# Kernel tuning notes

Measured on AMD Instinct MI355X. Metric: run time of the kernel, lower is better.

The kernel has to match this reference:

```python
import jax, jax.numpy as jnp
import numpy as np

D_MODEL = 1024
N_HEADS = 16
D_K = D_MODEL // N_HEADS
B, T = 4, 2048


def setup_inputs() -> dict:
    key = jax.random.key(0)
    ks = jax.random.split(key, 6)
    scale = 1.0 / np.sqrt(D_MODEL)
    q = jax.random.normal(ks[0], (B, T, D_MODEL), dtype=jnp.float32)
    # causal mask: True = masked / ignored (upper triangle)
    causal = jnp.triu(jnp.ones((T, T), dtype=bool), k=1)
    mask = jnp.broadcast_to(causal, (B, 1, T, T))
    Wq = jax.random.normal(ks[1], (D_MODEL, D_MODEL), dtype=jnp.float32) * scale
    Wk = jax.random.normal(ks[2], (D_MODEL, D_MODEL), dtype=jnp.float32) * scale
    Wv = jax.random.normal(ks[3], (D_MODEL, D_MODEL), dtype=jnp.float32) * scale
    Wo = jax.random.normal(ks[4], (D_MODEL, D_MODEL), dtype=jnp.float32) * scale
    bq = jnp.zeros((D_MODEL,), jnp.float32)
    bk = jnp.zeros((D_MODEL,), jnp.float32)
    bv = jnp.zeros((D_MODEL,), jnp.float32)
    bo = jnp.zeros((D_MODEL,), jnp.float32)
    return {"q": q, "mask": mask, "Wq": Wq, "bq": bq, "Wk": Wk, "bk": bk,
            "Wv": Wv, "bv": bv, "Wo": Wo, "bo": bo}


def reference(q, mask, Wq, bq, Wk, bk, Wv, bv, Wo, bo):
    # Self-attention: k = v = q (module defaults). Weights stored torch-style
    # (out, in): y = x @ W.T + b.
    b, tq, _ = q.shape
    qh = (q @ Wq.T + bq).reshape(b, tq, N_HEADS, D_K).transpose(0, 2, 1, 3)  # (B,H,T,dk)
    kh = (q @ Wk.T + bk).reshape(b, tq, N_HEADS, D_K).transpose(0, 2, 1, 3)
    vh = (q @ Wv.T + bv).reshape(b, tq, N_HEADS, D_K).transpose(0, 2, 1, 3)
    attn = jnp.einsum('bhqd,bhkd->bhqk', qh, kh) / np.sqrt(D_K).astype(np.float32)
    attn = jnp.where(mask, -jnp.inf, attn)
    attn = jax.nn.softmax(attn, axis=-1)
    out = jnp.einsum('bhqk,bhkd->bhqd', attn, vh)
    out = out.transpose(0, 2, 1, 3).reshape(b, tq, D_MODEL)
    return out @ Wo.T + bo
```

## Files before the change

### kernel.cpp

```cpp
#include <hip/hip_runtime.h>
#include <hip/hip_bf16.h>
#include <stdint.h>

#define D_MODEL 1024
#define NH      16
#define DKH     64
#define BATCH   4
#define SEQ     2048
#define MROWS   (BATCH*SEQ)

typedef __hip_bfloat16 bf16;
typedef __attribute__((ext_vector_type(8))) short  bf16x8;
typedef __attribute__((ext_vector_type(4))) short  bf16x4;
typedef __attribute__((ext_vector_type(4))) float  f32x4;
typedef __attribute__((ext_vector_type(2))) unsigned int u32x2;

#define CEXP 0.18033688011112042f

__device__ __forceinline__ bf16 f2bf(float x){ return __float2bfloat16(x); }

__device__ __forceinline__ void gload_lds16(const void* g, void* l) {
  __builtin_amdgcn_global_load_lds(
      (const __attribute__((address_space(1))) unsigned int*)g,
      (__attribute__((address_space(3))) unsigned int*)l, 16, 0, 0);
}

__device__ __forceinline__ unsigned int cvtpk(float lo, float hi) {
  unsigned int r;
  asm("v_cvt_pk_bf16_f32 %0, %1, %2" : "=v"(r) : "v"(lo), "v"(hi));
  return r;
}

#if __has_builtin(__builtin_amdgcn_mfma_f32_16x16x16bf16_1k)
#define MFMA16(a, b, c) __builtin_amdgcn_mfma_f32_16x16x16bf16_1k(a, b, c, 0, 0, 0)
#else
__device__ __forceinline__ f32x4 mfma16_asm(bf16x4 a, bf16x4 b, f32x4 c) {
  asm volatile("s_nop 2\n\t"
               "v_mfma_f32_16x16x16_bf16 %0, %1, %2, %0\n\t"
               "s_nop 7\n\ts_nop 2"
               : "+v"(c) : "v"(a), "v"(b));
  return c;
}
#define MFMA16(a, b, c) mfma16_asm(a, b, c)
#endif

__global__ __launch_bounds__(256)
void cvt_all(const float* __restrict__ q,
             const float* __restrict__ w0, const float* __restrict__ w1,
             const float* __restrict__ w2, const float* __restrict__ w3,
             bf16* __restrict__ qdst, bf16* __restrict__ wdst)
{
  const int NQB = (MROWS * D_MODEL) / 1024;
  const int bid = blockIdx.x;
  const float* src;
  bf16* dst;
  int i;
  if (bid < NQB) {
    src = q; dst = qdst;
    i = bid * 1024 + threadIdx.x * 4;
  } else {
    const int b2 = bid - NQB;
    const int w = b2 >> 10;
    src = (w == 0) ? w0 : (w == 1) ? w1 : (w == 2) ? w2 : w3;
    dst = wdst + (size_t)w * (D_MODEL * D_MODEL);
    i = (b2 & 1023) * 1024 + threadIdx.x * 4;
  }
  f32x4 v = *(const f32x4*)&src[i];
  union { bf16 e[4]; bf16x4 v4; } u;
  u.e[0] = f2bf(v[0]); u.e[1] = f2bf(v[1]);
  u.e[2] = f2bf(v[2]); u.e[3] = f2bf(v[3]);
  *(bf16x4*)&dst[i] = u.v4;
}

template <int MODE>
__global__ __launch_bounds__(512, 2)
void gemm8(const bf16* __restrict__ A, const bf16* __restrict__ W,
           const float* __restrict__ b0, const float* __restrict__ b1,
           const float* __restrict__ b2, void* __restrict__ Cbase)
{
  constexpr int K    = D_MODEL;
  constexpr int NT   = K / 64;
  constexpr int SLOT = (128 + 256) * 64;
  __shared__ __align__(16) short ring[3 * SLOT];

  const int tid  = threadIdx.x;
  const int lane = tid & 63;
  const int wave = tid >> 6;
  const int lm   = lane & 15;
  const int quad = lane >> 4;
  const int wm   = (wave >> 2) * 64;
  const int wn   = (wave & 3) * 64;
  const int bm   = blockIdx.x * 128;
  const int bn   = blockIdx.y * 256;

  const int rr    = tid >> 3;
  const int kperm = ((tid & 7) ^ (rr & 7)) * 8;
  const bf16* aS0 = A + (int64_t)(bm + rr) * K + kperm;
  const bf16* aS1 = aS0 + (int64_t)64 * K;
  const bf16* bS0 = W + (int64_t)(bn + rr) * K + kperm;
  const bf16* bS1 = bS0 + (int64_t)64 * K;
  const bf16* bS2 = bS0 + (int64_t)128 * K;
  const bf16* bS3 = bS0 + (int64_t)192 * K;

  f32x4 acc[4][4] = {};

#define STAGE8(T, S)                                                          \
  do {                                                                        \
    const int k0_ = (T) * 64;                                                 \
    short* As_ = &ring[(S) * SLOT];                                           \
    short* Bs_ = As_ + 128 * 64;                                              \
    gload_lds16(aS0 + k0_, &As_[tid * 8]);                                    \
    gload_lds16(aS1 + k0_, &As_[(tid + 512) * 8]);                            \
    gload_lds16(bS0 + k0_, &Bs_[tid * 8]);                                    \
    gload_lds16(bS1 + k0_, &Bs_[(tid + 512) * 8]);                            \
    gload_lds16(bS2 + k0_, &Bs_[(tid + 1024) * 8]);                           \
    gload_lds16(bS3 + k0_, &Bs_[(tid + 1536) * 8]);                           \
  } while (0)

  STAGE8(0, 0);
  STAGE8(1, 1);

#pragma unroll
  for (int t = 0; t < NT; ++t) {
    if (t < NT - 1) asm volatile("s_waitcnt vmcnt(6)" ::: "memory");
    else            asm volatile("s_waitcnt vmcnt(0)" ::: "memory");
    __builtin_amdgcn_s_barrier();
    asm volatile("" ::: "memory");
    if (t + 2 < NT) STAGE8(t + 2, (t + 2) % 3);

    const short* As = &ring[(t % 3) * SLOT];
    const short* Bs = As + 128 * 64;

    __builtin_amdgcn_s_setprio(1);
#pragma unroll
    for (int kk = 0; kk < 2; ++kk) {
      bf16x8 af[4], bfr[4];
#pragma unroll
      for (int i = 0; i < 4; ++i) {
        const int ra = wm + i * 16 + lm;
        af[i]  = *(const bf16x8*)&As[ra * 64 + (((kk * 4 + quad) ^ (ra & 7))) * 8];
        const int rb = wn + i * 16 + lm;
        bfr[i] = *(const bf16x8*)&Bs[rb * 64 + (((kk * 4 + quad) ^ (rb & 7))) * 8];
      }
#pragma unroll
      for (int i = 0; i < 4; ++i)
#pragma unroll
        for (int j = 0; j < 4; ++j)
          acc[i][j] = __builtin_amdgcn_mfma_f32_16x16x32_bf16(af[i], bfr[j], acc[i][j], 0, 0, 0);
    }
    __builtin_amdgcn_s_setprio(0);
  }
#undef STAGE8

  if constexpr (MODE == 1) {
    float* Cp = (float*)Cbase;
#pragma unroll
    for (int j = 0; j < 4; ++j) {
      const int n = bn + wn + j * 16 + lm;
      const float bv = b0[n];
#pragma unroll
      for (int i = 0; i < 4; ++i)
#pragma unroll
        for (int r = 0; r < 4; ++r) {
          const int m = bm + wm + i * 16 + quad * 4 + r;
          Cp[(int64_t)m * D_MODEL + n] = acc[i][j][r] + bv;
        }
    }
  } else {
    const int proj = bn >> 10;
    const int nl0  = bn & 1023;
    const float* bias = (proj == 0) ? b0 : (proj == 1) ? b1 : b2;
    if (proj == 2) {
      bf16* Vt = (bf16*)Cbase + 2 * (size_t)MROWS * D_MODEL;
#pragma unroll
      for (int j = 0; j < 4; ++j) {
        const int nl = nl0 + wn + j * 16 + lm;
        const float bv = bias[nl];
#pragma unroll
        for (int i = 0; i < 4; ++i) {
          const int m0 = bm + wm + i * 16 + quad * 4;
          const int64_t base = (int64_t)((m0 >> 11) * 16 + (nl >> 6)) * (DKH * SEQ)
                             + (nl & 63) * SEQ + (m0 & 2047);
          union { bf16 e[4]; bf16x4 v4; } u;
#pragma unroll
          for (int r = 0; r < 4; ++r) u.e[r] = f2bf(acc[i][j][r] + bv);
          *(bf16x4*)&Vt[base] = u.v4;
        }
      }
    } else {
      bf16* Cp = (bf16*)Cbase + (size_t)proj * MROWS * D_MODEL;
      const float sc = (proj == 0) ? CEXP : 1.0f;
#pragma unroll
      for (int j = 0; j < 4; ++j) {
        const int nl = nl0 + wn + j * 16 + lm;
        const float bv = bias[nl];
#pragma unroll
        for (int i = 0; i < 4; ++i)
#pragma unroll
          for (int r = 0; r < 4; ++r) {
            const int m = bm + wm + i * 16 + quad * 4 + r;
            Cp[(int64_t)m * D_MODEL + nl] = f2bf((acc[i][j][r] + bv) * sc);
          }
      }
    }
  }
}

__global__ __launch_bounds__(256)
void attn_causal(const bf16* __restrict__ Q, const bf16* __restrict__ Kg,
                 const bf16* __restrict__ Vt, bf16* __restrict__ O)
{
  __shared__ __align__(16) short lK[2][64 * 64];
  __shared__ __align__(16) short lV[2][64 * 64];

  const int bid  = blockIdx.x;
  const int qt   = 31 - (bid >> 6);
  const int bh   = bid & 63;

  const int tid  = threadIdx.x;
  const int lane = tid & 63;
  const int wave = tid >> 6;
  const int lm   = lane & 15;
  const int quad = lane >> 4;
  const int qbase = qt * 64;
  const int64_t qkbase = (int64_t)((bh >> 4) * SEQ) * D_MODEL + (bh & 15) * DKH;
  const bf16* Kbase = Kg + qkbase;
  const bf16* Vbase = Vt + (int64_t)bh * DKH * SEQ;

  bf16x8 qf[2];
  {
    const bf16* qrow = Q + qkbase + (int64_t)(qbase + wave * 16 + lm) * D_MODEL;
    qf[0] = *(const bf16x8*)&qrow[quad * 8];
    qf[1] = *(const bf16x8*)&qrow[32 + quad * 8];
  }

  f32x4 o_acc[4] = {};
  f32x4 o_sum   = {};
  const bf16x4 ones4 = {16256, 16256, 16256, 16256};

  const int srow = tid >> 3;
  const int sg   = (tid & 7) ^ (srow & 7);
  const int wqv  = wave * 16 + lm;

  const bf16* kp0 = Kbase + (int64_t)srow        * D_MODEL + sg * 8;
  const bf16* kp1 = Kbase + (int64_t)(srow + 32) * D_MODEL + sg * 8;
  const bf16* vp0 = Vbase + (int64_t)srow        * SEQ + sg * 8;
  const bf16* vp1 = Vbase + (int64_t)(srow + 32) * SEQ + sg * 8;

#define STAGE(KB, BUF)                                                        \
  do {                                                                        \
    gload_lds16(kp0 + (int64_t)(KB) * D_MODEL, &lK[BUF][tid * 8]);            \
    gload_lds16(kp1 + (int64_t)(KB) * D_MODEL, &lK[BUF][(tid + 256) * 8]);    \
    gload_lds16(vp0 + (KB), &lV[BUF][tid * 8]);                               \
    gload_lds16(vp1 + (KB), &lV[BUF][(tid + 256) * 8]);                       \
  } while (0)

  STAGE(0, 0);

  for (int kt = 0; kt <= qt; ++kt) {
    const int cur = kt & 1;
    __syncthreads();
    if (kt < qt) STAGE((kt + 1) * 64, cur ^ 1);

    const short* lKc = lK[cur];
    const short* lVc = lV[cur];

    f32x4 s[4];
    __builtin_amdgcn_s_setprio(1);
#pragma unroll
    for (int ni = 0; ni < 4; ++ni) {
      const int row = ni * 16 + lm;
      f32x4 zz = {};
      bf16x8 k0 = *(const bf16x8*)&lKc[row * 64 + ((quad       ^ (row & 7))) * 8];
      bf16x8 k1 = *(const bf16x8*)&lKc[row * 64 + (((4 + quad) ^ (row & 7))) * 8];
      zz = __builtin_amdgcn_mfma_f32_16x16x32_bf16(k0, qf[0], zz, 0, 0, 0);
      zz = __builtin_amdgcn_mfma_f32_16x16x32_bf16(k1, qf[1], zz, 0, 0, 0);
      s[ni] = zz;
    }
    __builtin_amdgcn_s_setprio(0);

    if (kt == qt) {
#pragma unroll
      for (int ni = 0; ni < 4; ++ni) {
        const int kp = ni * 16 + quad * 4;
#pragma unroll
        for (int r = 0; r < 4; ++r)
          if (kp + r > wqv) s[ni][r] = -1e30f;
      }
    }

    bf16x4 pk[4];
#pragma unroll
    for (int ni = 0; ni < 4; ++ni) {
      const float p0 = __builtin_amdgcn_exp2f(s[ni][0]);
      const float p1 = __builtin_amdgcn_exp2f(s[ni][1]);
      const float p2 = __builtin_amdgcn_exp2f(s[ni][2]);
      const float p3 = __builtin_amdgcn_exp2f(s[ni][3]);
      union { unsigned int u[2]; bf16x4 v; } pu;
      pu.u[0] = cvtpk(p0, p1);
      pu.u[1] = cvtpk(p2, p3);
      pk[ni] = pu.v;
    }

    __builtin_amdgcn_s_setprio(1);
#pragma unroll
    for (int ni = 0; ni < 4; ++ni) {
      o_sum = MFMA16(pk[ni], ones4, o_sum);
#pragma unroll
      for (int di = 0; di < 4; ++di) {
        const int vrow = di * 16 + lm;
        const bf16x4 vb = *(const bf16x4*)&lVc[vrow * 64
            + (((ni * 2 + (quad >> 1)) ^ (vrow & 7))) * 8 + (quad & 1) * 4];
        o_acc[di] = MFMA16(pk[ni], vb, o_acc[di]);
      }
    }
    __builtin_amdgcn_s_setprio(0);
  }
#undef STAGE

  float lr[4];
#pragma unroll
  for (int r = 0; r < 4; ++r) lr[r] = 1.0f / o_sum[r];

#pragma unroll
  for (int di = 0; di < 4; ++di)
#pragma unroll
    for (int r = 0; r < 4; ++r) {
      const int qrow = qbase + wave * 16 + quad * 4 + r;
      O[qkbase + (int64_t)qrow * D_MODEL + di * 16 + lm] = f2bf(o_acc[di][r] * lr[r]);
    }
}

extern "C" void kernel_launch(void* const* d_in, const int* in_sizes, int n_in,
                              void* d_out, int out_size, void* d_ws, size_t ws_size,
                              hipStream_t stream)
{
  const float* q  = (const float*)d_in[0];
  const float* Wq = (const float*)d_in[2];
  const float* bq = (const float*)d_in[3];
  const float* Wk = (const float*)d_in[4];
  const float* bk = (const float*)d_in[5];
  const float* Wv = (const float*)d_in[6];
  const float* bv = (const float*)d_in[7];
  const float* Wo = (const float*)d_in[8];
  const float* bo = (const float*)d_in[9];
  float* out = (float*)d_out;

  const size_t NQ = (size_t)MROWS * D_MODEL;
  const size_t NW = (size_t)D_MODEL * D_MODEL;

  bf16* qb  = (bf16*)d_ws;
  bf16* Wb  = qb + NQ;
  bf16* Qw  = Wb + 4 * NW;
  bf16* Kw  = Qw + NQ;
  bf16* Vtw = Kw + NQ;

  cvt_all<<<dim3(NQ / 1024 + 4 * NW / 1024), 256, 0, stream>>>(
      q, Wq, Wk, Wv, Wo, qb, Wb);

  gemm8<0><<<dim3(MROWS / 128, 3 * D_MODEL / 256), 512, 0, stream>>>(
      qb, Wb, bq, bk, bv, Qw);

  attn_causal<<<dim3(BATCH * NH * (SEQ / 64)), 256, 0, stream>>>(Qw, Kw, Vtw, qb);

  gemm8<1><<<dim3(MROWS / 128, D_MODEL / 256), 512, 0, stream>>>(
      qb, Wb + 3 * NW, bo, bo, bo, out);
}
```

Baseline: 277.9 us.

## Use 16x16x32 MFMA for PV with permuted V staging; interleave GEMM prefetch

The attention PV product switches from pairs of 16x16x16 MFMAs to single 16x16x32 MFMAs by concatenating two P fragments. V tiles are now staged with 4-byte global-to-LDS loads in a permuted layout so that each lane's 8-wide V fragment matches the concatenated P k-ordering. The GEMM main loop splits its next-stage prefetch across the two k-substeps, adding a barrier and lgkmcnt wait before each MFMA block. The aim is to halve the MFMA instruction count in the PV phase and spread the load issue in the GEMM, at the cost of many more small V loads and extra barriers.

Result: faster. 264.3 us (-4.9%).

```diff
diff --git a/kernel.cpp b/kernel.cpp
--- a/kernel.cpp
+++ b/kernel.cpp
@@ -24,25 +24,17 @@
       (const __attribute__((address_space(1))) unsigned int*)g,
       (__attribute__((address_space(3))) unsigned int*)l, 16, 0, 0);
 }
+__device__ __forceinline__ void gload_lds4(const void* g, void* l) {
+  __builtin_amdgcn_global_load_lds(
+      (const __attribute__((address_space(1))) unsigned int*)g,
+      (__attribute__((address_space(3))) unsigned int*)l, 4, 0, 0);
+}
 
 __device__ __forceinline__ unsigned int cvtpk(float lo, float hi) {
   unsigned int r;
   asm("v_cvt_pk_bf16_f32 %0, %1, %2" : "=v"(r) : "v"(lo), "v"(hi));
   return r;
 }
-
-#if __has_builtin(__builtin_amdgcn_mfma_f32_16x16x16bf16_1k)
-#define MFMA16(a, b, c) __builtin_amdgcn_mfma_f32_16x16x16bf16_1k(a, b, c, 0, 0, 0)
-#else
-__device__ __forceinline__ f32x4 mfma16_asm(bf16x4 a, bf16x4 b, f32x4 c) {
-  asm volatile("s_nop 2\n\t"
-               "v_mfma_f32_16x16x16_bf16 %0, %1, %2, %0\n\t"
-               "s_nop 7\n\ts_nop 2"
-               : "+v"(c) : "v"(a), "v"(b));
-  return c;
-}
-#define MFMA16(a, b, c) mfma16_asm(a, b, c)
-#endif
 
 __global__ __launch_bounds__(256)
 void cvt_all(const float* __restrict__ q,
@@ -126,12 +118,14 @@
     else            asm volatile("s_waitcnt vmcnt(0)" ::: "memory");
     __builtin_amdgcn_s_barrier();
     asm volatile("" ::: "memory");
-    if (t + 2 < NT) STAGE8(t + 2, (t + 2) % 3);
 
     const short* As = &ring[(t % 3) * SLOT];
     const short* Bs = As + 128 * 64;
-
-    __builtin_amdgcn_s_setprio(1);
+    short* Ad = &ring[((t + 2) % 3) * SLOT];
+    short* Bd = Ad + 128 * 64;
+    const bool dost = (t + 2 < NT);
+    const int k2 = (t + 2) * 64;
+
 #pragma unroll
     for (int kk = 0; kk < 2; ++kk) {
       bf16x8 af[4], bfr[4];
@@ -142,13 +136,28 @@
         const int rb = wn + i * 16 + lm;
         bfr[i] = *(const bf16x8*)&Bs[rb * 64 + (((kk * 4 + quad) ^ (rb & 7))) * 8];
       }
+      if (dost) {
+        if (kk == 0) {
+          gload_lds16(aS0 + k2, &Ad[tid * 8]);
+          gload_lds16(aS1 + k2, &Ad[(tid + 512) * 8]);
+          gload_lds16(bS0 + k2, &Bd[tid * 8]);
+        } else {
+          gload_lds16(bS1 + k2, &Bd[(tid + 512) * 8]);
+          gload_lds16(bS2 + k2, &Bd[(tid + 1024) * 8]);
+          gload_lds16(bS3 + k2, &Bd[(tid + 1536) * 8]);
+        }
+      }
+      __builtin_amdgcn_s_barrier();
+      asm volatile("s_waitcnt lgkmcnt(0)" ::: "memory");
+      __builtin_amdgcn_sched_barrier(0);
+      __builtin_amdgcn_s_setprio(1);
 #pragma unroll
       for (int i = 0; i < 4; ++i)
 #pragma unroll
         for (int j = 0; j < 4; ++j)
           acc[i][j] = __builtin_amdgcn_mfma_f32_16x16x32_bf16(af[i], bfr[j], acc[i][j], 0, 0, 0);
-    }
-    __builtin_amdgcn_s_setprio(0);
+      __builtin_amdgcn_s_setprio(0);
+    }
   }
 #undef STAGE8
 
@@ -236,7 +245,8 @@
 
   f32x4 o_acc[4] = {};
   f32x4 o_sum   = {};
-  const bf16x4 ones4 = {16256, 16256, 16256, 16256};
+  const bf16x8 ones8 = {16256, 16256, 16256, 16256,
+                        16256, 16256, 16256, 16256};
 
   const int srow = tid >> 3;
   const int sg   = (tid & 7) ^ (srow & 7);
@@ -244,15 +254,20 @@
 
   const bf16* kp0 = Kbase + (int64_t)srow        * D_MODEL + sg * 8;
   const bf16* kp1 = Kbase + (int64_t)(srow + 32) * D_MODEL + sg * 8;
-  const bf16* vp0 = Vbase + (int64_t)srow        * SEQ + sg * 8;
-  const bf16* vp1 = Vbase + (int64_t)(srow + 32) * SEQ + sg * 8;
+
+  const int u5   = tid & 31;
+  const int Gv   = (u5 >> 2) ^ (tid >> 5);
+  const int koff = 32 * (Gv >> 2) + (Gv & 3) * 4
+                 + ((u5 & 1) << 1) + ((u5 & 2) << 3);
+  const bf16* vpp = Vbase + (int64_t)(tid >> 5) * SEQ + koff;
 
 #define STAGE(KB, BUF)                                                        \
   do {                                                                        \
     gload_lds16(kp0 + (int64_t)(KB) * D_MODEL, &lK[BUF][tid * 8]);            \
     gload_lds16(kp1 + (int64_t)(KB) * D_MODEL, &lK[BUF][(tid + 256) * 8]);    \
-    gload_lds16(vp0 + (KB), &lV[BUF][tid * 8]);                               \
-    gload_lds16(vp1 + (KB), &lV[BUF][(tid + 256) * 8]);                       \
+    _Pragma("unroll")                                                         \
+    for (int c = 0; c < 8; ++c)                                               \
+      gload_lds4(vpp + (KB) + c * 8 * SEQ, &lV[BUF][c * 512 + tid * 2]);      \
   } while (0)
 
   STAGE(0, 0);
@@ -289,29 +304,30 @@
       }
     }
 
-    bf16x4 pk[4];
+    unsigned int pku[4][2];
 #pragma unroll
     for (int ni = 0; ni < 4; ++ni) {
       const float p0 = __builtin_amdgcn_exp2f(s[ni][0]);
       const float p1 = __builtin_amdgcn_exp2f(s[ni][1]);
       const float p2 = __builtin_amdgcn_exp2f(s[ni][2]);
       const float p3 = __builtin_amdgcn_exp2f(s[ni][3]);
-      union { unsigned int u[2]; bf16x4 v; } pu;
-      pu.u[0] = cvtpk(p0, p1);
-      pu.u[1] = cvtpk(p2, p3);
-      pk[ni] = pu.v;
+      pku[ni][0] = cvtpk(p0, p1);
+      pku[ni][1] = cvtpk(p2, p3);
     }
 
     __builtin_amdgcn_s_setprio(1);
 #pragma unroll
-    for (int ni = 0; ni < 4; ++ni) {
-      o_sum = MFMA16(pk[ni], ones4, o_sum);
+    for (int m = 0; m < 2; ++m) {
+      union { unsigned int u[4]; bf16x8 v; } au;
+      au.u[0] = pku[2 * m][0];     au.u[1] = pku[2 * m][1];
+      au.u[2] = pku[2 * m + 1][0]; au.u[3] = pku[2 * m + 1][1];
+      o_sum = __builtin_amdgcn_mfma_f32_16x16x32_bf16(au.v, ones8, o_sum, 0, 0, 0);
 #pragma unroll
       for (int di = 0; di < 4; ++di) {
         const int vrow = di * 16 + lm;
-        const bf16x4 vb = *(const bf16x4*)&lVc[vrow * 64
-            + (((ni * 2 + (quad >> 1)) ^ (vrow & 7))) * 8 + (quad & 1) * 4];
-        o_acc[di] = MFMA16(pk[ni], vb, o_acc[di]);
+        const bf16x8 vb = *(const bf16x8*)&lVc[vrow * 64
+            + (((m * 4 + quad) ^ (vrow & 7))) * 8];
+        o_acc[di] = __builtin_amdgcn_mfma_f32_16x16x32_bf16(au.v, vb, o_acc[di], 0, 0, 0);
       }
     }
     __builtin_amdgcn_s_setprio(0);
```
